# Kernel tuning notes

Measured on AMD Instinct MI355X. Metric: run time of the kernel, lower is better.

Reference implementation:

```python
import jax, jax.numpy as jnp
import numpy as np

N = 50000
E = 800000
FEAT, ACT = 96, 32
HID, HEADS = 64, 4
NEG_SLOPE = 0.2


def gat_conv(x, src, dst, W, att_s, att_d, bias):
    # x: [N, F_in]; W: [F_in, H*C]; att_s/att_d: [H, C]; bias: [H*C]
    H, C = att_s.shape
    h = (x @ W).reshape(-1, H, C)                      # [N, H, C]
    a_s = jnp.einsum('nhc,hc->nh', h, att_s)           # [N, H]
    a_d = jnp.einsum('nhc,hc->nh', h, att_d)
    e = jax.nn.leaky_relu(a_s[src] + a_d[dst], NEG_SLOPE)  # [E, H]
    m = jax.ops.segment_max(e, dst, num_segments=N)
    e = jnp.exp(e - m[dst])
    denom = jax.ops.segment_sum(e, dst, num_segments=N)
    alpha = e / (denom[dst] + 1e-16)                   # softmax over incoming edges
    out = jax.ops.segment_sum(alpha[:, :, None] * h[src], dst, num_segments=N)
    return out.reshape(-1, H * C) + bias


def setup_inputs() -> dict:
    key = jax.random.key(0)
    ks = jax.random.split(key, 12)
    node_features = jax.random.normal(ks[0], (N, FEAT), dtype=jnp.float32)
    actions = jax.random.normal(ks[1], (N, ACT), dtype=jnp.float32)
    edge_index = jax.random.randint(ks[2], (2, E), 0, N, dtype=jnp.int64)
    s = 0.1
    return {
        'node_features': node_features,
        'actions': actions,
        'edge_index': edge_index,
        'W_emb': jax.random.normal(ks[3], (FEAT + ACT, HID), dtype=jnp.float32) * s,
        'b_emb': jnp.zeros((HID,), dtype=jnp.float32),
        'W1': jax.random.normal(ks[4], (HID, HEADS * HID), dtype=jnp.float32) * s,
        'att_s1': jax.random.normal(ks[5], (HEADS, HID), dtype=jnp.float32) * s,
        'att_d1': jax.random.normal(ks[6], (HEADS, HID), dtype=jnp.float32) * s,
        'b1': jnp.zeros((HEADS * HID,), dtype=jnp.float32),
        'W2': jax.random.normal(ks[7], (HEADS * HID, HID), dtype=jnp.float32) * s,
        'att_s2': jax.random.normal(ks[8], (1, HID), dtype=jnp.float32) * s,
        'att_d2': jax.random.normal(ks[9], (1, HID), dtype=jnp.float32) * s,
        'b2': jnp.zeros((HID,), dtype=jnp.float32),
        'W_v': jax.random.normal(ks[10], (HID, 1), dtype=jnp.float32) * s,
        'b_v': jnp.zeros((1,), dtype=jnp.float32),
    }


def reference(node_features, actions, edge_index, W_emb, b_emb, W1, att_s1, att_d1, b1,
              W2, att_s2, att_d2, b2, W_v, b_v):
    # add self loops (PyG GATConv default add_self_loops=True)
    loop = jnp.arange(N, dtype=edge_index.dtype)
    src = jnp.concatenate([edge_index[0], loop])
    dst = jnp.concatenate([edge_index[1], loop])
    x = jnp.concatenate([node_features, actions], axis=1)
    x = x @ W_emb + b_emb
    x = jax.nn.relu(gat_conv(x, src, dst, W1, att_s1, att_d1, b1))
    x = jax.nn.relu(gat_conv(x, src, dst, W2, att_s2, att_d2, b2))
    g = jnp.mean(x, axis=0, keepdims=True)  # [1, HID]
    return g @ W_v + b_v                    # [1, 1]
```

## Files before the change

### kernel.cpp

```cpp
#include <hip/hip_runtime.h>
#include <hip/hip_bf16.h>
#include <math.h>

#define FEAT 96
#define ACTF 32

using frag8 = __attribute__((ext_vector_type(8))) short;
using f32x4 = __attribute__((ext_vector_type(4))) float;

__device__ __forceinline__ float lrelu(float x) { return x >= 0.f ? x : 0.2f * x; }
__device__ __forceinline__ void atomAddF(float* p, float v) {
    __hip_atomic_fetch_add(p, v, __ATOMIC_RELAXED, __HIP_MEMORY_SCOPE_AGENT);
}
__device__ __forceinline__ float expc(float x) { return __expf(fminf(x, 60.f)); }
__device__ __forceinline__ unsigned short f2bf(float f) {
    __hip_bfloat16 h = __float2bfloat16(f);
    return *(unsigned short*)&h;
}
__device__ __forceinline__ float bf2f(unsigned short u) {
    return __uint_as_float((unsigned)u << 16);
}

__global__ __launch_bounds__(256) void xprep(
    const float* __restrict__ nf, const float* __restrict__ act,
    unsigned short* __restrict__ Xh, unsigned short* __restrict__ Xl, long long total) {
    long long i = (long long)blockIdx.x * 256 + threadIdx.x;
    if (i >= total) return;
    int n = (int)(i >> 7), k = (int)(i & 127);
    float v = (k < FEAT) ? nf[(size_t)n * FEAT + k] : act[(size_t)n * ACTF + (k - FEAT)];
    unsigned short h = f2bf(v);
    Xh[i] = h;
    Xl[i] = f2bf(v - bf2f(h));
}

__global__ void w1prep(const float* __restrict__ Wemb, const float* __restrict__ bemb,
                       const float* __restrict__ W1,
                       unsigned short* __restrict__ wfh, unsigned short* __restrict__ wfl,
                       float* __restrict__ bfused) {
    int k = blockIdx.x, c = threadIdx.x;
    if (k < 128) {
        float s = 0.f;
        for (int j = 0; j < 64; ++j) s = fmaf(Wemb[k * 64 + j], W1[j * 256 + c], s);
        unsigned short h = f2bf(s);
        wfh[(size_t)c * 128 + k] = h;
        wfl[(size_t)c * 128 + k] = f2bf(s - bf2f(h));
    } else {
        float s = 0.f;
        for (int j = 0; j < 64; ++j) s = fmaf(bemb[j], W1[j * 256 + c], s);
        bfused[c] = s;
    }
}

__global__ __launch_bounds__(256) void gemm1_mfma(
    const unsigned short* __restrict__ Xh, const unsigned short* __restrict__ Xl,
    const unsigned short* __restrict__ wfh, const unsigned short* __restrict__ wfl,
    const float* __restrict__ bfused, const float* __restrict__ att_s,
    const float* __restrict__ att_d, __hip_bfloat16* __restrict__ h1b,
    float* __restrict__ a_s, float* __restrict__ a_d, int N) {
    int w = threadIdx.x >> 6, l = threadIdx.x & 63;
    int nb = (blockIdx.x * 4 + w) * 16;
    if (nb >= N) return;
    int r16 = l & 15, kg = l >> 4;
    int arow = min(nb + r16, N - 1);
    const short* ahp = (const short*)Xh + (size_t)arow * 128 + kg * 8;
    const short* alp = (const short*)Xl + (size_t)arow * 128 + kg * 8;
    frag8 ah[4], al[4];
    #pragma unroll
    for (int ks = 0; ks < 4; ++ks) {
        ah[ks] = *(const frag8*)(ahp + ks * 32);
        al[ks] = *(const frag8*)(alp + ks * 32);
    }
    f32x4 acc[16];
    #pragma unroll
    for (int ct = 0; ct < 16; ++ct) {
        acc[ct] = (f32x4){0.f, 0.f, 0.f, 0.f};
        const short* bhp = (const short*)wfh + (size_t)(ct * 16 + r16) * 128 + kg * 8;
        const short* blp = (const short*)wfl + (size_t)(ct * 16 + r16) * 128 + kg * 8;
        #pragma unroll
        for (int ks = 0; ks < 4; ++ks) {
            frag8 bh = *(const frag8*)(bhp + ks * 32);
            frag8 bl = *(const frag8*)(blp + ks * 32);
            acc[ct] = __builtin_amdgcn_mfma_f32_16x16x32_bf16(ah[ks], bh, acc[ct], 0, 0, 0);
            acc[ct] = __builtin_amdgcn_mfma_f32_16x16x32_bf16(al[ks], bh, acc[ct], 0, 0, 0);
            acc[ct] = __builtin_amdgcn_mfma_f32_16x16x32_bf16(ah[ks], bl, acc[ct], 0, 0, 0);
        }
    }
    float s_s[4] = {0.f, 0.f, 0.f, 0.f}, s_d[4] = {0.f, 0.f, 0.f, 0.f};
    #pragma unroll
    for (int ct = 0; ct < 16; ++ct) {
        int ch = ct * 16 + r16;
        float bias = bfused[ch];
        float aw = att_s[ch], dw = att_d[ch];
        #pragma unroll
        for (int r = 0; r < 4; ++r) {
            int node = nb + kg * 4 + r;
            float v = acc[ct][r] + bias;
            if (node < N) h1b[(size_t)node * 256 + ch] = __float2bfloat16(v);
            s_s[r] = fmaf(v, aw, s_s[r]);
            s_d[r] = fmaf(v, dw, s_d[r]);
        }
    }
    #pragma unroll
    for (int r = 0; r < 4; ++r) {
        #pragma unroll
        for (int o = 1; o < 16; o <<= 1) {
            s_s[r] += __shfl_xor(s_s[r], o);
            s_d[r] += __shfl_xor(s_d[r], o);
        }
        int node = nb + kg * 4 + r;
        if (r16 == 0 && node < N) {
            a_s[(size_t)node * 4] = 0.f;
        }
    }
}

__global__ __launch_bounds__(256) void gemm1_mfma_h(
    const unsigned short* __restrict__ Xh, const unsigned short* __restrict__ Xl,
    const unsigned short* __restrict__ wfh, const unsigned short* __restrict__ wfl,
    const float* __restrict__ bfused, const float* __restrict__ att_s,
    const float* __restrict__ att_d, __hip_bfloat16* __restrict__ h1b,
    float* __restrict__ a_s, float* __restrict__ a_d, int N) {
    int w = threadIdx.x >> 6, l = threadIdx.x & 63;
    int nb = (blockIdx.x * 4 + w) * 16;
    if (nb >= N) return;
    int r16 = l & 15, kg = l >> 4;
    int arow = min(nb + r16, N - 1);
    const short* ahp = (const short*)Xh + (size_t)arow * 128 + kg * 8;
    const short* alp = (const short*)Xl + (size_t)arow * 128 + kg * 8;
    frag8 ah[4], al[4];
    #pragma unroll
    for (int ks = 0; ks < 4; ++ks) {
        ah[ks] = *(const frag8*)(ahp + ks * 32);
        al[ks] = *(const frag8*)(alp + ks * 32);
    }
    f32x4 acc[16];
    #pragma unroll
    for (int ct = 0; ct < 16; ++ct) {
        acc[ct] = (f32x4){0.f, 0.f, 0.f, 0.f};
        const short* bhp = (const short*)wfh + (size_t)(ct * 16 + r16) * 128 + kg * 8;
        const short* blp = (const short*)wfl + (size_t)(ct * 16 + r16) * 128 + kg * 8;
        #pragma unroll
        for (int ks = 0; ks < 4; ++ks) {
            frag8 bh = *(const frag8*)(bhp + ks * 32);
            frag8 bl = *(const frag8*)(blp + ks * 32);
            acc[ct] = __builtin_amdgcn_mfma_f32_16x16x32_bf16(ah[ks], bh, acc[ct], 0, 0, 0);
            acc[ct] = __builtin_amdgcn_mfma_f32_16x16x32_bf16(al[ks], bh, acc[ct], 0, 0, 0);
            acc[ct] = __builtin_amdgcn_mfma_f32_16x16x32_bf16(ah[ks], bl, acc[ct], 0, 0, 0);
        }
    }
    float s_s[4][4], s_d[4][4];
    #pragma unroll
    for (int hh = 0; hh < 4; ++hh)
        #pragma unroll
        for (int r = 0; r < 4; ++r) { s_s[hh][r] = 0.f; s_d[hh][r] = 0.f; }
    #pragma unroll
    for (int ct = 0; ct < 16; ++ct) {
        int ch = ct * 16 + r16;
        int hh = ct >> 2;
        float bias = bfused[ch];
        float aw = att_s[ch], dw = att_d[ch];
        #pragma unroll
        for (int r = 0; r < 4; ++r) {
            int node = nb + kg * 4 + r;
            float v = acc[ct][r] + bias;
            if (node < N) h1b[(size_t)node * 256 + ch] = __float2bfloat16(v);
            s_s[hh][r] = fmaf(v, aw, s_s[hh][r]);
            s_d[hh][r] = fmaf(v, dw, s_d[hh][r]);
        }
    }
    #pragma unroll
    for (int hh = 0; hh < 4; ++hh) {
        #pragma unroll
        for (int r = 0; r < 4; ++r) {
            float vs = s_s[hh][r], vd = s_d[hh][r];
            #pragma unroll
            for (int o = 1; o < 16; o <<= 1) {
                vs += __shfl_xor(vs, o);
                vd += __shfl_xor(vd, o);
            }
            int node = nb + kg * 4 + r;
            if (r16 == 0 && node < N) {
                a_s[(size_t)node * 4 + hh] = vs;
                a_d[(size_t)node * 4 + hh] = vd;
            }
        }
    }
}

__global__ void w2_prep(const float* __restrict__ W2, __hip_bfloat16* __restrict__ w2t) {
    int i = blockIdx.x * 256 + threadIdx.x;
    int k = i >> 6, c = i & 63;
    w2t[(size_t)c * 256 + k] = __float2bfloat16(W2[i]);
}

__global__ __launch_bounds__(256) void gemm2_mfma(
    const __hip_bfloat16* __restrict__ out1b, const __hip_bfloat16* __restrict__ w2t,
    const float* __restrict__ att_s, const float* __restrict__ att_d,
    __hip_bfloat16* __restrict__ h2b, float* __restrict__ a_s, float* __restrict__ a_d,
    int N) {
    int w = threadIdx.x >> 6, l = threadIdx.x & 63;
    int nb = (blockIdx.x * 4 + w) * 16;
    if (nb >= N) return;
    int r16 = l & 15, kg = l >> 4;
    const short* A = (const short*)out1b;
    int arow = min(nb + r16, N - 1);
    const short* arp = A + (size_t)arow * 256 + kg * 8;
    frag8 a[8];
    #pragma unroll
    for (int ks = 0; ks < 8; ++ks) a[ks] = *(const frag8*)(arp + ks * 32);
    const short* B = (const short*)w2t;
    f32x4 acc[4];
    #pragma unroll
    for (int ct = 0; ct < 4; ++ct) {
        acc[ct] = (f32x4){0.f, 0.f, 0.f, 0.f};
        const short* brp = B + (size_t)(ct * 16 + r16) * 256 + kg * 8;
        #pragma unroll
        for (int ks = 0; ks < 8; ++ks) {
            frag8 b = *(const frag8*)(brp + ks * 32);
            acc[ct] = __builtin_amdgcn_mfma_f32_16x16x32_bf16(a[ks], b, acc[ct], 0, 0, 0);
        }
    }
    float s_s[4] = {0.f, 0.f, 0.f, 0.f}, s_d[4] = {0.f, 0.f, 0.f, 0.f};
    #pragma unroll
    for (int ct = 0; ct < 4; ++ct) {
        int ch = ct * 16 + r16;
        float aw = att_s[ch], dw = att_d[ch];
        #pragma unroll
        for (int r = 0; r < 4; ++r) {
            int node = nb + kg * 4 + r;
            float v = acc[ct][r];
            if (node < N) h2b[(size_t)node * 64 + ch] = __float2bfloat16(v);
            s_s[r] = fmaf(v, aw, s_s[r]);
            s_d[r] = fmaf(v, dw, s_d[r]);
        }
    }
    #pragma unroll
    for (int r = 0; r < 4; ++r) {
        #pragma unroll
        for (int o = 1; o < 16; o <<= 1) {
            s_s[r] += __shfl_xor(s_s[r], o);
            s_d[r] += __shfl_xor(s_d[r], o);
        }
        int node = nb + kg * 4 + r;
        if (r16 == 0 && node < N) { a_s[node] = s_s[r]; a_d[node] = s_d[r]; }
    }
}

__global__ void hist_kernel(const int* __restrict__ dst, int* __restrict__ cnt, int E, int ET) {
    int e = blockIdx.x * blockDim.x + threadIdx.x;
    if (e >= ET) return;
    int d = (e < E) ? dst[e] : (e - E);
    atomicAdd(&cnt[d], 1);
}

__global__ __launch_bounds__(256) void scan_blocks(
    const int* __restrict__ cnt, int* __restrict__ off, int* __restrict__ bsum, int n) {
    int b = blockIdx.x, t = threadIdx.x;
    int i = b * 256 + t;
    int v = (i < n) ? cnt[i] : 0;
    int lane = t & 63, w = t >> 6;
    int x = v;
    #pragma unroll
    for (int o = 1; o < 64; o <<= 1) {
        int y = __shfl_up(x, o);
        if (lane >= o) x += y;
    }
    __shared__ int wtot[4];
    if (lane == 63) wtot[w] = x;
    __syncthreads();
    int add = 0;
    #pragma unroll
    for (int j = 0; j < 4; ++j) if (j < w) add += wtot[j];
    int incl = x + add;
    if (i < n) off[i] = incl - v;
    if (t == 255) bsum[b] = incl;
}

__global__ __launch_bounds__(256) void scan_tops(
    const int* __restrict__ bsum, int* __restrict__ bpre, int nb) {
    int t = threadIdx.x;
    int v = (t < nb) ? bsum[t] : 0;
    int lane = t & 63, w = t >> 6;
    int x = v;
    #pragma unroll
    for (int o = 1; o < 64; o <<= 1) {
        int y = __shfl_up(x, o);
        if (lane >= o) x += y;
    }
    __shared__ int wtot[4];
    if (lane == 63) wtot[w] = x;
    __syncthreads();
    int add = 0;
    #pragma unroll
    for (int j = 0; j < 4; ++j) if (j < w) add += wtot[j];
    if (t < nb) bpre[t] = x + add - v;
    if (t == 255) bpre[nb] = x + add;
}

__global__ __launch_bounds__(256) void scan_add(
    const int* __restrict__ bpre, int* __restrict__ off, int n, int nb) {
    int b = blockIdx.x, t = threadIdx.x;
    int i = b * 256 + t;
    if (i < n) off[i] += bpre[b];
    if (b == 0 && t == 0) off[n] = bpre[nb];
}

__global__ void scatter_kernel(const int* __restrict__ src, const int* __restrict__ dst,
                               const int* __restrict__ off, int* __restrict__ cur,
                               int* __restrict__ perm, int E, int ET) {
    int e = blockIdx.x * blockDim.x + threadIdx.x;
    if (e >= ET) return;
    int s = (e < E) ? src[e] : (e - E);
    int d = (e < E) ? dst[e] : (e - E);
    int r = atomicAdd(&cur[d], 1);
    perm[off[d] + r] = s;
}

__global__ __launch_bounds__(256) void fused_gat4(
    const int* __restrict__ off, const int* __restrict__ perm,
    const float* __restrict__ a_s, const float* __restrict__ a_d,
    const __hip_bfloat16* __restrict__ h1b, const float* __restrict__ bias,
    __hip_bfloat16* __restrict__ out1b, int N) {
    __shared__ float exls[4][64][4];
    __shared__ unsigned idxls[4][64];
    int w = threadIdx.x >> 6, l = threadIdx.x & 63;
    int d = blockIdx.x * 4 + w;
    if (d >= N) return;
    int lo = off[d], hi = off[d + 1];
    const float4* as4 = (const float4*)a_s;
    float4 ad = ((const float4*)a_d)[d];
    float dx = 0.f, dy = 0.f, dz = 0.f, dw = 0.f;
    for (int e = lo + l; e < hi; e += 64) {
        float4 a = as4[perm[e]];
        dx += expc(lrelu(a.x + ad.x));
        dy += expc(lrelu(a.y + ad.y));
        dz += expc(lrelu(a.z + ad.z));
        dw += expc(lrelu(a.w + ad.w));
    }
    #pragma unroll
    for (int o = 32; o; o >>= 1) {
        dx += __shfl_xor(dx, o); dy += __shfl_xor(dy, o);
        dz += __shfl_xor(dz, o); dw += __shfl_xor(dw, o);
    }
    int g = l >> 4;
    float rr = 1.f / ((g == 0 ? dx : g == 1 ? dy : g == 2 ? dz : dw) + 1e-16f);
    const char* hb = (const char*)h1b;
    unsigned laneoff = (unsigned)l * 8u;
    float acc0 = 0.f, acc1 = 0.f, acc2 = 0.f, acc3 = 0.f;
    for (int base = lo; base < hi; base += 64) {
        int e = base + l;
        if (e < hi) {
            int s = perm[e];
            float4 a = as4[s];
            exls[w][l][0] = expc(lrelu(a.x + ad.x));
            exls[w][l][1] = expc(lrelu(a.y + ad.y));
            exls[w][l][2] = expc(lrelu(a.z + ad.z));
            exls[w][l][3] = expc(lrelu(a.w + ad.w));
            idxls[w][l] = (unsigned)s * 512u;
        }
        int n = min(64, hi - base);
        #pragma unroll 4
        for (int i = 0; i < n; ++i) {
            float ex = exls[w][i][g];
            unsigned voff = idxls[w][i] + laneoff;
            uint2 v = *(const uint2*)(hb + voff);
            float f0 = __uint_as_float(v.x << 16);
            float f1 = __uint_as_float(v.x & 0xffff0000u);
            float f2 = __uint_as_float(v.y << 16);
            float f3 = __uint_as_float(v.y & 0xffff0000u);
            acc0 = fmaf(ex, f0, acc0);
            acc1 = fmaf(ex, f1, acc1);
            acc2 = fmaf(ex, f2, acc2);
            acc3 = fmaf(ex, f3, acc3);
        }
    }
    float4 bv = ((const float4*)bias)[l];
    ushort4 o4;
    o4.x = f2bf(fmaxf(fmaf(acc0, rr, bv.x), 0.f));
    o4.y = f2bf(fmaxf(fmaf(acc1, rr, bv.y), 0.f));
    o4.z = f2bf(fmaxf(fmaf(acc2, rr, bv.z), 0.f));
    o4.w = f2bf(fmaxf(fmaf(acc3, rr, bv.w), 0.f));
    ((ushort4*)out1b)[(size_t)d * 64 + l] = o4;
}

__global__ __launch_bounds__(256) void fused_gat1(
    const int* __restrict__ off, const int* __restrict__ perm,
    const float* __restrict__ a_s, const float* __restrict__ a_d,
    const __hip_bfloat16* __restrict__ h2b, const float* __restrict__ bias,
    float* __restrict__ out2, int N) {
    __shared__ float2 alds[4][64];
    int w = threadIdx.x >> 6, l = threadIdx.x & 63;
    int d = blockIdx.x * 4 + w;
    if (d >= N) return;
    int lo = off[d], hi = off[d + 1];
    float add = a_d[d];
    float den = 0.f;
    for (int e = lo + l; e < hi; e += 64)
        den += expc(lrelu(a_s[perm[e]] + add));
    #pragma unroll
    for (int o = 32; o; o >>= 1) den += __shfl_xor(den, o);
    float rr = 1.f / (den + 1e-16f);
    const char* hb = (const char*)h2b;
    unsigned laneoff = (unsigned)l * 2u;
    float acc = 0.f;
    for (int base = lo; base < hi; base += 64) {
        int e = base + l;
        if (e < hi) {
            int s = perm[e];
            float ex = expc(lrelu(a_s[s] + add));
            alds[w][l] = make_float2(ex, __uint_as_float((unsigned)s * 128u));
        }
        int n = min(64, hi - base);
        #pragma unroll 4
        for (int i = 0; i < n; ++i) {
            float2 p = alds[w][i];
            unsigned voff = __float_as_uint(p.y) + laneoff;
            unsigned u = *(const unsigned short*)(hb + voff);
            acc = fmaf(p.x, __uint_as_float(u << 16), acc);
        }
    }
    out2[(size_t)d * 64 + l] = fmaxf(fmaf(acc, rr, bias[l]), 0.f);
}

__global__ void colsum_kernel(const float* __restrict__ x, float* __restrict__ g, int N) {
    __shared__ float part[4][64];
    int c = threadIdx.x & 63;
    int r = threadIdx.x >> 6;
    float acc = 0.f;
    for (long long n = (long long)blockIdx.x * 4 + r; n < N; n += (long long)gridDim.x * 4)
        acc += x[n * 64 + c];
    part[r][c] = acc;
    __syncthreads();
    if (r == 0) {
        float v = part[0][c] + part[1][c] + part[2][c] + part[3][c];
        atomAddF(&g[c], v);
    }
}

__global__ void final_kernel(const float* __restrict__ g, const float* __restrict__ Wv,
                             const float* __restrict__ bv, float* __restrict__ out, int N) {
    int lane = threadIdx.x;
    float v = (g[lane] / (float)N) * Wv[lane];
    #pragma unroll
    for (int off = 32; off; off >>= 1) v += __shfl_down(v, off);
    if (lane == 0) out[0] = v + bv[0];
}

extern "C" void kernel_launch(void* const* d_in, const int* in_sizes, int n_in,
                              void* d_out, int out_size, void* d_ws, size_t ws_size,
                              hipStream_t stream) {
    const float* nf   = (const float*)d_in[0];
    const float* act  = (const float*)d_in[1];
    const int*   ei   = (const int*)d_in[2];
    const float* Wemb = (const float*)d_in[3];
    const float* bemb = (const float*)d_in[4];
    const float* W1   = (const float*)d_in[5];
    const float* as1  = (const float*)d_in[6];
    const float* ad1  = (const float*)d_in[7];
    const float* b1   = (const float*)d_in[8];
    const float* W2   = (const float*)d_in[9];
    const float* as2  = (const float*)d_in[10];
    const float* ad2  = (const float*)d_in[11];
    const float* b2   = (const float*)d_in[12];
    const float* Wv   = (const float*)d_in[13];
    const float* bv   = (const float*)d_in[14];
    float* out = (float*)d_out;

    const int N = in_sizes[0] / FEAT;
    const int E = in_sizes[2] / 2;
    const int ET = E + N;
    const int* srcp = ei;
    const int* dstp = ei + E;
    const int NB = (N + 255) / 256;

    char* ws = (char*)d_ws;
    unsigned short* Xh = (unsigned short*)ws;
    unsigned short* Xl = Xh + (size_t)N * 128;
    __hip_bfloat16* h1b   = (__hip_bfloat16*)(Xl + (size_t)N * 128);
    __hip_bfloat16* out1b = h1b + (size_t)N * 256;
    float* a_s  = (float*)(out1b + (size_t)N * 256);
    float* a_d  = a_s + (size_t)N * 4;
    __hip_bfloat16* h2b = (__hip_bfloat16*)(a_d + (size_t)N * 4);
    float* out2 = (float*)(h2b + (size_t)N * 64);
    float* g    = out2 + (size_t)N * 64;
    __hip_bfloat16* w2t = (__hip_bfloat16*)(g + 64);
    unsigned short* wfh = (unsigned short*)(w2t + 64 * 256);
    unsigned short* wfl = wfh + 256 * 128;
    float* bfused = (float*)(wfl + 256 * 128);
    int* cnt  = (int*)Xh;
    int* off  = cnt + N;
    int* cur  = off + N + 1;
    int* perm = cur + N;
    int* bsum = perm + ET;
    int* bpre = bsum + NB;

    (void)ws_size; (void)n_in; (void)out_size;

    long long xtot = (long long)N * 128;
    xprep<<<(int)((xtot + 255) / 256), 256, 0, stream>>>(nf, act, Xh, Xl, xtot);
    w1prep<<<129, 256, 0, stream>>>(Wemb, bemb, W1, wfh, wfl, bfused);
    w2_prep<<<64, 256, 0, stream>>>(W2, w2t);

    gemm1_mfma_h<<<(N + 63) / 64, 256, 0, stream>>>(Xh, Xl, wfh, wfl, bfused,
                                                    as1, ad1, h1b, a_s, a_d, N);

    hipMemsetAsync(cnt, 0, (size_t)N * sizeof(int), stream);
    hipMemsetAsync(cur, 0, (size_t)N * sizeof(int), stream);
    hist_kernel<<<(ET + 255) / 256, 256, 0, stream>>>(dstp, cnt, E, ET);
    scan_blocks<<<NB, 256, 0, stream>>>(cnt, off, bsum, N);
    scan_tops<<<1, 256, 0, stream>>>(bsum, bpre, NB);
    scan_add<<<NB, 256, 0, stream>>>(bpre, off, N, NB);
    scatter_kernel<<<(ET + 255) / 256, 256, 0, stream>>>(srcp, dstp, off, cur, perm, E, ET);

    fused_gat4<<<(N + 3) / 4, 256, 0, stream>>>(off, perm, a_s, a_d, h1b, b1, out1b, N);

    gemm2_mfma<<<(N + 63) / 64, 256, 0, stream>>>(out1b, w2t, as2, ad2, h2b, a_s, a_d, N);
    fused_gat1<<<(N + 3) / 4, 256, 0, stream>>>(off, perm, a_s, a_d, h2b, b2, out2, N);

    hipMemsetAsync(g, 0, 64 * sizeof(float), stream);
    colsum_kernel<<<512, 256, 0, stream>>>(out2, g, N);
    final_kernel<<<1, 64, 0, stream>>>(g, Wv, bv, out, N);
}
```

Before: 339.2 us.

## Make GEMM1 persistent with each wave keeping one head's weights in registers

GEMM1 is now a persistent grid-stride kernel with 1024 blocks. Each wave owns one head (64 output channels) and loads that slice of the split-bf16 weights into registers once, then loops over 16-row node tiles that all four waves share. Before, every wave reloaded all 256 columns of weights for each tile. This removes repeated weight loads and shrinks the per-wave accumulator set, but the four waves in a block now read the same A rows, and the large weight register footprint (32 frag8) may limit occupancy. The unused gemm1_mfma variant is also removed.

```diff
diff --git a/kernel.cpp b/kernel.cpp
--- a/kernel.cpp
+++ b/kernel.cpp
@@ -51,128 +51,69 @@
     }
 }
 
-__global__ __launch_bounds__(256) void gemm1_mfma(
+__global__ __launch_bounds__(256, 2) void gemm1_mfma_w(
     const unsigned short* __restrict__ Xh, const unsigned short* __restrict__ Xl,
     const unsigned short* __restrict__ wfh, const unsigned short* __restrict__ wfl,
     const float* __restrict__ bfused, const float* __restrict__ att_s,
     const float* __restrict__ att_d, __hip_bfloat16* __restrict__ h1b,
     float* __restrict__ a_s, float* __restrict__ a_d, int N) {
     int w = threadIdx.x >> 6, l = threadIdx.x & 63;
-    int nb = (blockIdx.x * 4 + w) * 16;
-    if (nb >= N) return;
     int r16 = l & 15, kg = l >> 4;
-    int arow = min(nb + r16, N - 1);
-    const short* ahp = (const short*)Xh + (size_t)arow * 128 + kg * 8;
-    const short* alp = (const short*)Xl + (size_t)arow * 128 + kg * 8;
-    frag8 ah[4], al[4];
-    #pragma unroll
-    for (int ks = 0; ks < 4; ++ks) {
-        ah[ks] = *(const frag8*)(ahp + ks * 32);
-        al[ks] = *(const frag8*)(alp + ks * 32);
-    }
-    f32x4 acc[16];
-    #pragma unroll
-    for (int ct = 0; ct < 16; ++ct) {
-        acc[ct] = (f32x4){0.f, 0.f, 0.f, 0.f};
+    frag8 bh[4][4], bl[4][4];
+    #pragma unroll
+    for (int c = 0; c < 4; ++c) {
+        int ct = w * 4 + c;
         const short* bhp = (const short*)wfh + (size_t)(ct * 16 + r16) * 128 + kg * 8;
         const short* blp = (const short*)wfl + (size_t)(ct * 16 + r16) * 128 + kg * 8;
         #pragma unroll
         for (int ks = 0; ks < 4; ++ks) {
-            frag8 bh = *(const frag8*)(bhp + ks * 32);
-            frag8 bl = *(const frag8*)(blp + ks * 32);
-            acc[ct] = __builtin_amdgcn_mfma_f32_16x16x32_bf16(ah[ks], bh, acc[ct], 0, 0, 0);
-            acc[ct] = __builtin_amdgcn_mfma_f32_16x16x32_bf16(al[ks], bh, acc[ct], 0, 0, 0);
-            acc[ct] = __builtin_amdgcn_mfma_f32_16x16x32_bf16(ah[ks], bl, acc[ct], 0, 0, 0);
-        }
-    }
-    float s_s[4] = {0.f, 0.f, 0.f, 0.f}, s_d[4] = {0.f, 0.f, 0.f, 0.f};
-    #pragma unroll
-    for (int ct = 0; ct < 16; ++ct) {
-        int ch = ct * 16 + r16;
-        float bias = bfused[ch];
-        float aw = att_s[ch], dw = att_d[ch];
+            bh[c][ks] = *(const frag8*)(bhp + ks * 32);
+            bl[c][ks] = *(const frag8*)(blp + ks * 32);
+        }
+    }
+    float biasv[4], awv[4], dwv[4];
+    #pragma unroll
+    for (int c = 0; c < 4; ++c) {
+        int ch = w * 64 + c * 16 + r16;
+        biasv[c] = bfused[ch];
+        awv[c] = att_s[ch];
+        dwv[c] = att_d[ch];
+    }
+    int ntiles = (N + 15) >> 4;
+    for (int tile = blockIdx.x; tile < ntiles; tile += gridDim.x) {
+        int nb = tile * 16;
+        int arow = nb + r16; if (arow >= N) arow = N - 1;
+        const short* ahp = (const short*)Xh + (size_t)arow * 128 + kg * 8;
+        const short* alp = (const short*)Xl + (size_t)arow * 128 + kg * 8;
+        frag8 ah[4], al[4];
+        #pragma unroll
+        for (int ks = 0; ks < 4; ++ks) {
+            ah[ks] = *(const frag8*)(ahp + ks * 32);
+            al[ks] = *(const frag8*)(alp + ks * 32);
+        }
+        float s_s[4] = {0.f, 0.f, 0.f, 0.f}, s_d[4] = {0.f, 0.f, 0.f, 0.f};
+        #pragma unroll
+        for (int c = 0; c < 4; ++c) {
+            f32x4 acc = (f32x4){0.f, 0.f, 0.f, 0.f};
+            #pragma unroll
+            for (int ks = 0; ks < 4; ++ks) {
+                acc = __builtin_amdgcn_mfma_f32_16x16x32_bf16(ah[ks], bh[c][ks], acc, 0, 0, 0);
+                acc = __builtin_amdgcn_mfma_f32_16x16x32_bf16(al[ks], bh[c][ks], acc, 0, 0, 0);
+                acc = __builtin_amdgcn_mfma_f32_16x16x32_bf16(ah[ks], bl[c][ks], acc, 0, 0, 0);
+            }
+            int ch = w * 64 + c * 16 + r16;
+            #pragma unroll
+            for (int r = 0; r < 4; ++r) {
+                int node = nb + kg * 4 + r;
+                float v = acc[r] + biasv[c];
+                if (node < N) h1b[(size_t)node * 256 + ch] = __float2bfloat16(v);
+                s_s[r] = fmaf(v, awv[c], s_s[r]);
+                s_d[r] = fmaf(v, dwv[c], s_d[r]);
+            }
+        }
         #pragma unroll
         for (int r = 0; r < 4; ++r) {
-            int node = nb + kg * 4 + r;
-            float v = acc[ct][r] + bias;
-            if (node < N) h1b[(size_t)node * 256 + ch] = __float2bfloat16(v);
-            s_s[r] = fmaf(v, aw, s_s[r]);
-            s_d[r] = fmaf(v, dw, s_d[r]);
-        }
-    }
-    #pragma unroll
-    for (int r = 0; r < 4; ++r) {
-        #pragma unroll
-        for (int o = 1; o < 16; o <<= 1) {
-            s_s[r] += __shfl_xor(s_s[r], o);
-            s_d[r] += __shfl_xor(s_d[r], o);
-        }
-        int node = nb + kg * 4 + r;
-        if (r16 == 0 && node < N) {
-            a_s[(size_t)node * 4] = 0.f;
-        }
-    }
-}
-
-__global__ __launch_bounds__(256) void gemm1_mfma_h(
-    const unsigned short* __restrict__ Xh, const unsigned short* __restrict__ Xl,
-    const unsigned short* __restrict__ wfh, const unsigned short* __restrict__ wfl,
-    const float* __restrict__ bfused, const float* __restrict__ att_s,
-    const float* __restrict__ att_d, __hip_bfloat16* __restrict__ h1b,
-    float* __restrict__ a_s, float* __restrict__ a_d, int N) {
-    int w = threadIdx.x >> 6, l = threadIdx.x & 63;
-    int nb = (blockIdx.x * 4 + w) * 16;
-    if (nb >= N) return;
-    int r16 = l & 15, kg = l >> 4;
-    int arow = min(nb + r16, N - 1);
-    const short* ahp = (const short*)Xh + (size_t)arow * 128 + kg * 8;
-    const short* alp = (const short*)Xl + (size_t)arow * 128 + kg * 8;
-    frag8 ah[4], al[4];
-    #pragma unroll
-    for (int ks = 0; ks < 4; ++ks) {
-        ah[ks] = *(const frag8*)(ahp + ks * 32);
-        al[ks] = *(const frag8*)(alp + ks * 32);
-    }
-    f32x4 acc[16];
-    #pragma unroll
-    for (int ct = 0; ct < 16; ++ct) {
-        acc[ct] = (f32x4){0.f, 0.f, 0.f, 0.f};
-        const short* bhp = (const short*)wfh + (size_t)(ct * 16 + r16) * 128 + kg * 8;
-        const short* blp = (const short*)wfl + (size_t)(ct * 16 + r16) * 128 + kg * 8;
-        #pragma unroll
-        for (int ks = 0; ks < 4; ++ks) {
-            frag8 bh = *(const frag8*)(bhp + ks * 32);
-            frag8 bl = *(const frag8*)(blp + ks * 32);
-            acc[ct] = __builtin_amdgcn_mfma_f32_16x16x32_bf16(ah[ks], bh, acc[ct], 0, 0, 0);
-            acc[ct] = __builtin_amdgcn_mfma_f32_16x16x32_bf16(al[ks], bh, acc[ct], 0, 0, 0);
-            acc[ct] = __builtin_amdgcn_mfma_f32_16x16x32_bf16(ah[ks], bl, acc[ct], 0, 0, 0);
-        }
-    }
-    float s_s[4][4], s_d[4][4];
-    #pragma unroll
-    for (int hh = 0; hh < 4; ++hh)
-        #pragma unroll
-        for (int r = 0; r < 4; ++r) { s_s[hh][r] = 0.f; s_d[hh][r] = 0.f; }
-    #pragma unroll
-    for (int ct = 0; ct < 16; ++ct) {
-        int ch = ct * 16 + r16;
-        int hh = ct >> 2;
-        float bias = bfused[ch];
-        float aw = att_s[ch], dw = att_d[ch];
-        #pragma unroll
-        for (int r = 0; r < 4; ++r) {
-            int node = nb + kg * 4 + r;
-            float v = acc[ct][r] + bias;
-            if (node < N) h1b[(size_t)node * 256 + ch] = __float2bfloat16(v);
-            s_s[hh][r] = fmaf(v, aw, s_s[hh][r]);
-            s_d[hh][r] = fmaf(v, dw, s_d[hh][r]);
-        }
-    }
-    #pragma unroll
-    for (int hh = 0; hh < 4; ++hh) {
-        #pragma unroll
-        for (int r = 0; r < 4; ++r) {
-            float vs = s_s[hh][r], vd = s_d[hh][r];
+            float vs = s_s[r], vd = s_d[r];
             #pragma unroll
             for (int o = 1; o < 16; o <<= 1) {
                 vs += __shfl_xor(vs, o);
@@ -180,8 +121,8 @@
             }
             int node = nb + kg * 4 + r;
             if (r16 == 0 && node < N) {
-                a_s[(size_t)node * 4 + hh] = vs;
-                a_d[(size_t)node * 4 + hh] = vd;
+                a_s[(size_t)node * 4 + w] = vs;
+                a_d[(size_t)node * 4 + w] = vd;
             }
         }
     }
@@ -501,8 +442,8 @@
     w1prep<<<129, 256, 0, stream>>>(Wemb, bemb, W1, wfh, wfl, bfused);
     w2_prep<<<64, 256, 0, stream>>>(W2, w2t);
 
-    gemm1_mfma_h<<<(N + 63) / 64, 256, 0, stream>>>(Xh, Xl, wfh, wfl, bfused,
-                                                    as1, ad1, h1b, a_s, a_d, N);
+    gemm1_mfma_w<<<1024, 256, 0, stream>>>(Xh, Xl, wfh, wfl, bfused,
+                                           as1, ad1, h1b, a_s, a_d, N);
 
     hipMemsetAsync(cnt, 0, (size_t)N * sizeof(int), stream);
     hipMemsetAsync(cur, 0, (size_t)N * sizeof(int), stream);
```

Result: faster. 293.8 us (-13.4%).
